# Performance work log

Measured on AMD Instinct MI355X. Metric: run time of the kernel, lower is better.

The kernel has to match this reference:

```python
import jax, jax.numpy as jnp
import numpy as np

B, S, HID = 2, 1024, 2048
NH, NKV, D = 16, 8, 128
EPS = 1e-4 / 65535.0  # observer eps from ConcatObserver


def _ste(x, dq):
    # straight-through estimator used by torch fake-quant
    return x + jax.lax.stop_gradient(dq - x)


def _fq_range(x, mn, mx):
    # 16-bit per-tensor affine quantize-dequantize over a given range
    scale = jnp.maximum((mx - mn) / 65535.0, EPS)
    zp = jnp.round(-mn / scale)
    q = jnp.clip(jnp.round(x / scale) + zp, 0.0, 65535.0)
    return _ste(x, (q - zp) * scale)


def fq16(x):
    # ActivationQDQ(bits=16), per-tensor affine, zero included in range
    mn = jnp.minimum(jnp.min(x), 0.0)
    mx = jnp.maximum(jnp.max(x), 0.0)
    return _fq_range(x, mn, mx)


def fq8_sym(x):
    # ActivationQDQ(bits=8, per_tensor_symmetric)
    scale = jnp.maximum(jnp.max(jnp.abs(x)) / 127.0, 1e-12)
    q = jnp.clip(jnp.round(x / scale), -128.0, 127.0)
    return _ste(x, q * scale)


def lpbq_linear(x, W, block=32, qmax=7.0):
    # QLinearLPBQ: int4 weights with per-(out, block-of-32-inputs) scales, no bias
    O, I = W.shape
    Wb = W.reshape(O, I // block, block)
    s = jnp.maximum(jnp.max(jnp.abs(Wb), axis=-1, keepdims=True) / qmax, 1e-12)
    Wq = (jnp.clip(jnp.round(Wb / s), -qmax - 1.0, qmax) * s).reshape(O, I)
    return x @ _ste(W, Wq).T


def rmsnorm_fq(x, w, eps=1e-6):
    # QRMSNorm(head_dim, quant_bits=16)
    var = jnp.mean(x * x, axis=-1, keepdims=True)
    return fq16(x * jax.lax.rsqrt(var + eps) * w)


def rotate_half_fq(x):
    # rotate_half with neg-half QDQ and concat observer (range = union of observed tensors)
    d = x.shape[-1] // 2
    x1, x2 = x[..., :d], x[..., d:]
    neg = fq16(-x2)
    mn = jnp.minimum(jnp.minimum(jnp.min(x), jnp.min(neg)), 0.0)
    mx = jnp.maximum(jnp.maximum(jnp.max(x), jnp.max(neg)), 0.0)
    return _fq_range(jnp.concatenate([neg, x1], axis=-1), mn, mx)


def _attn_forward(hidden_states, cos, sin, attention_mask, Wq, Wk, Wv, Wo, q_norm_w, k_norm_w):
    scaling = D ** -0.5
    hs = fq16(hidden_states)                                            # q_proj_input_qdq
    q = fq16(lpbq_linear(hs, Wq)).reshape(B, S, NH, D)                  # q_norm_input_qdq
    q = jnp.transpose(rmsnorm_fq(q, q_norm_w), (0, 2, 1, 3))            # [B,NH,S,D]
    k = fq16(lpbq_linear(hs, Wk)).reshape(B, S, NKV, D)                 # k_norm_input_qdq
    k = jnp.transpose(rmsnorm_fq(k, k_norm_w), (0, 2, 1, 3))            # [B,NKV,S,D]
    v = jnp.transpose(lpbq_linear(hs, Wv).reshape(B, S, NKV, D), (0, 2, 1, 3))
    q = fq16(q)                                                         # q_norm_output_qdq
    k = fq16(k)                                                         # k_norm_output_qdq
    c = cos[:, None, :, :]
    s_ = sin[:, None, :, :]
    q = fq16(fq16(q * c) + fq16(rotate_half_fq(q) * s_))                # q RoPE with QDQs
    k = fq16(fq16(k * c) + fq16(rotate_half_fq(k) * s_))                # k RoPE with QDQs
    k = fq8_sym(k)                                                      # k_cast_to_int8_qdq
    v = fq8_sym(fq16(v))                                                # v int16 then int8 QDQ
    k = jnp.repeat(k, NH // NKV, axis=1)                                # repeat_kv
    v = jnp.repeat(v, NH // NKV, axis=1)
    sc = fq16(jnp.full((1,), scaling, dtype=hs.dtype))                  # scaling_qdq
    attn = fq16(fq16(jnp.einsum('bhsd,bhtd->bhst', q, k)) * sc)         # qk_matmul + mul_0
    amin = fq16(jnp.min(attn, axis=-1, keepdims=True))                  # reduce_min_output_qdq
    vv = fq16(amin + fq16(jnp.full((1,), -20.0, dtype=hs.dtype)))       # minus_0 (+ neg_20)
    attn = fq16(jnp.where(attention_mask == 0, attn, vv))               # where_attn_qdq
    attn = fq16(jax.nn.softmax(attn.astype(jnp.float32), axis=-1).astype(hs.dtype))
    out = fq16(jnp.einsum('bhst,bhtd->bhsd', attn, v))                  # attn_value_matmul
    out = jnp.transpose(out, (0, 2, 1, 3)).reshape(B, S, NH * D)
    return lpbq_linear(out, Wo), attn


def setup_inputs() -> dict:
    key = jax.random.key(0)
    ks = jax.random.split(key, 6)
    hidden_states = jax.random.normal(ks[0], (B, S, HID), jnp.float32)
    pos = jnp.arange(S, dtype=jnp.float32)
    inv_freq = 1.0 / (1e6 ** (jnp.arange(0, D, 2, dtype=jnp.float32) / D))
    fr = pos[:, None] * inv_freq[None, :]
    emb = jnp.concatenate([fr, fr], axis=-1)                            # [S, D]
    cos = jnp.broadcast_to(jnp.cos(emb)[None], (B, S, D))
    sin = jnp.broadcast_to(jnp.sin(emb)[None], (B, S, D))
    attention_mask = jnp.triu(jnp.ones((S, S), jnp.int32), 1)[None, None]  # 0=keep (causal)
    Wq = jax.random.normal(ks[1], (NH * D, HID), jnp.float32) * 0.02
    Wk = jax.random.normal(ks[2], (NKV * D, HID), jnp.float32) * 0.02
    Wv = jax.random.normal(ks[3], (NKV * D, HID), jnp.float32) * 0.02
    Wo = jax.random.normal(ks[4], (HID, NH * D), jnp.float32) * 0.02
    q_norm_w = jnp.ones((D,), jnp.float32)
    k_norm_w = jnp.ones((D,), jnp.float32)
    return {"hidden_states": hidden_states, "cos": cos, "sin": sin,
            "attention_mask": attention_mask, "Wq": Wq, "Wk": Wk, "Wv": Wv, "Wo": Wo,
            "q_norm_w": q_norm_w, "k_norm_w": k_norm_w}


def reference(hidden_states, cos, sin, attention_mask, Wq, Wk, Wv, Wo, q_norm_w, k_norm_w):
    return _attn_forward(hidden_states, cos, sin, attention_mask, Wq, Wk, Wv, Wo, q_norm_w, k_norm_w)
```

## Files before the change

### kernel.cpp

```cpp
#include <hip/hip_runtime.h>
#include <cfloat>
#include <cmath>


#define FQ_EPS      1.5259021896696422e-09f
#define SCALING_F   0.08838834764831845f
#define S_LEN       1024

typedef _Float16 h8_t __attribute__((ext_vector_type(8)));
typedef _Float16 h4_t __attribute__((ext_vector_type(4)));
typedef float    f4_t __attribute__((ext_vector_type(4)));
typedef unsigned short u16x4 __attribute__((ext_vector_type(4)));

__device__ __forceinline__ unsigned f2o(float f){
  unsigned u = __float_as_uint(f);
  return (u & 0x80000000u) ? ~u : (u | 0x80000000u);
}
__device__ __forceinline__ float o2f(unsigned u){
  return __uint_as_float((u & 0x80000000u) ? (u ^ 0x80000000u) : ~u);
}
__device__ __forceinline__ float dec_slot(const unsigned* st, int s){ return o2f(st[s*16]); }

struct FQP { float scale, zp, inv; };
__device__ __forceinline__ FQP fqp_raw(float mn, float mx){
  FQP p; p.scale = fmaxf((mx - mn)/65535.0f, FQ_EPS); p.zp = rintf(-mn/p.scale);
  p.inv = 1.0f/p.scale; return p;
}
__device__ __forceinline__ FQP fqp(float mn0, float mx0){
  return fqp_raw(fminf(mn0, 0.0f), fmaxf(mx0, 0.0f));
}
__device__ __forceinline__ float fqa(float x, FQP p){
  float q = rintf(x*p.inv) + p.zp;
  q = fminf(fmaxf(q, 0.0f), 65535.0f);
  return (q - p.zp)*p.scale;
}
__device__ __forceinline__ float fq8(float x, float s, float si){
  return fminf(fmaxf(rintf(x*si), -128.0f), 127.0f)*s;
}

__device__ __forceinline__ float bred_min(float v, float* red){
  int tid = threadIdx.x; red[tid] = v; __syncthreads();
  for (int s = 128; s > 0; s >>= 1){ if (tid < s) red[tid] = fminf(red[tid], red[tid+s]); __syncthreads(); }
  float r = red[0]; __syncthreads(); return r;
}
__device__ __forceinline__ float bred_max(float v, float* red){
  int tid = threadIdx.x; red[tid] = v; __syncthreads();
  for (int s = 128; s > 0; s >>= 1){ if (tid < s) red[tid] = fmaxf(red[tid], red[tid+s]); __syncthreads(); }
  float r = red[0]; __syncthreads(); return r;
}


__global__ void k_init(unsigned* stats){
  int i = blockIdx.x*blockDim.x + threadIdx.x;
  if (i < 1024) stats[i] = (((i & 15) == 0) && (((i >> 4) & 1) == 0)) ? 0xFFFFFFFFu : 0u;
}

__global__ __launch_bounds__(256) void k_quantw4(const float* __restrict__ Wq, const float* __restrict__ Wk,
                                                 const float* __restrict__ Wv, const float* __restrict__ Wo,
                                                 _Float16* __restrict__ Qh, _Float16* __restrict__ Kh,
                                                 _Float16* __restrict__ Vh, _Float16* __restrict__ Oh){
  int bx = blockIdx.x;
  const float* W; _Float16* Wh; int base;
  if (bx < 4096){ W = Wq; Wh = Qh; base = 0; }
  else if (bx < 6144){ W = Wk; Wh = Kh; base = 4096; }
  else if (bx < 8192){ W = Wv; Wh = Vh; base = 6144; }
  else { W = Wo; Wh = Oh; base = 8192; }
  int i = (bx - base)*256 + threadIdx.x;
  float4 v = ((const float4*)W)[i];
  float am = fmaxf(fmaxf(fabsf(v.x), fabsf(v.y)), fmaxf(fabsf(v.z), fabsf(v.w)));
  #pragma unroll
  for (int m = 1; m < 8; m <<= 1) am = fmaxf(am, __shfl_xor(am, m, 64));
  float s = fmaxf(am/7.0f, 1e-12f), si = 1.0f/s;
  h4_t o;
  o[0] = (_Float16)(fminf(fmaxf(rintf(v.x*si), -8.0f), 7.0f)*s);
  o[1] = (_Float16)(fminf(fmaxf(rintf(v.y*si), -8.0f), 7.0f)*s);
  o[2] = (_Float16)(fminf(fmaxf(rintf(v.z*si), -8.0f), 7.0f)*s);
  o[3] = (_Float16)(fminf(fmaxf(rintf(v.w*si), -8.0f), 7.0f)*s);
  *(h4_t*)(Wh + ((size_t)i << 2)) = o;
}

__global__ __launch_bounds__(256) void k_minmax(const float* __restrict__ x, int n, unsigned* stats, int slot){
  float mn = FLT_MAX, mx = -FLT_MAX;
  for (int i = blockIdx.x*256 + threadIdx.x; i < n; i += gridDim.x*256){
    float v = x[i]; mn = fminf(mn, v); mx = fmaxf(mx, v);
  }
  __shared__ float red[256];
  float bmn = bred_min(mn, red), bmx = bred_max(mx, red);
  if (threadIdx.x == 0){ atomicMin(&stats[slot*16], f2o(bmn)); atomicMax(&stats[(slot+1)*16], f2o(bmx)); }
}

__global__ __launch_bounds__(256) void k_fq_ew16(const float* __restrict__ x, _Float16* __restrict__ y,
                                                 const unsigned* stats, int slot){
  FQP p = fqp(dec_slot(stats, slot), dec_slot(stats, slot+1));
  int i = blockIdx.x*256 + threadIdx.x;
  float4 v = ((const float4*)x)[i];
  h4_t o;
  o[0] = (_Float16)fqa(v.x, p); o[1] = (_Float16)fqa(v.y, p);
  o[2] = (_Float16)fqa(v.z, p); o[3] = (_Float16)fqa(v.w, p);
  *(h4_t*)(y + ((size_t)i << 2)) = o;
}

__global__ __launch_bounds__(256) void k_fq_qk(const float* __restrict__ qbuf, const float* __restrict__ kbuf,
                                               _Float16* __restrict__ q_h, _Float16* __restrict__ k_h,
                                               const unsigned* stats){
  int bx = blockIdx.x;
  if (bx < 4096){
    FQP p = fqp(dec_slot(stats, 24), dec_slot(stats, 25));
    int i = bx*256 + threadIdx.x;
    float4 v = ((const float4*)qbuf)[i];
    h4_t o;
    o[0] = (_Float16)fqa(v.x, p); o[1] = (_Float16)fqa(v.y, p);
    o[2] = (_Float16)fqa(v.z, p); o[3] = (_Float16)fqa(v.w, p);
    *(h4_t*)(q_h + ((size_t)i << 2)) = o;
  } else {
    FQP p = fqp(dec_slot(stats, 26), dec_slot(stats, 27));
    float lo = fqa(dec_slot(stats, 26), p), hi = fqa(dec_slot(stats, 27), p);
    float s8 = fmaxf(fmaxf(fabsf(lo), fabsf(hi))/127.0f, 1e-12f), s8i = 1.0f/s8;
    int i = (bx - 4096)*256 + threadIdx.x;
    float4 v = ((const float4*)kbuf)[i];
    h4_t o;
    o[0] = (_Float16)fq8(fqa(v.x, p), s8, s8i); o[1] = (_Float16)fq8(fqa(v.y, p), s8, s8i);
    o[2] = (_Float16)fq8(fqa(v.z, p), s8, s8i); o[3] = (_Float16)fq8(fqa(v.w, p), s8, s8i);
    *(h4_t*)(k_h + ((size_t)i << 2)) = o;
  }
}

#define GLDS16(g, l) __builtin_amdgcn_global_load_lds( \
    (__attribute__((address_space(1))) unsigned int*)(g), \
    (__attribute__((address_space(3))) unsigned int*)(l), 16, 0, 0)

__device__ __forceinline__ void stage_tile(const _Float16* __restrict__ src, int ld, int k0,
                                           _Float16* __restrict__ dst){
  #pragma unroll
  for (int it = 0; it < 2; it++){
    int c = threadIdx.x + (it << 8);
    int row = c >> 2, off = (c & 3) << 3;
    GLDS16(src + (size_t)row*ld + k0 + off, dst + (c << 3));
  }
}

__device__ __forceinline__ void hgemm_main(const _Float16* __restrict__ A, int lda,
                                           const _Float16* __restrict__ B, int ldb, int K,
                                           f4_t acc[4][4], _Float16* As, _Float16* Bs){
  int lane = threadIdx.x & 63, wave = threadIdx.x >> 6;
  int wm = wave & 1, wn = wave >> 1, quad = lane >> 4, l15 = lane & 15;
  for (int k0 = 0; k0 < K; k0 += 32){
    __syncthreads();
    stage_tile(A, lda, k0, As);
    stage_tile(B, ldb, k0, Bs);
    __syncthreads();
    h8_t af[4], bf[4];
    #pragma unroll
    for (int mt = 0; mt < 4; mt++)
      af[mt] = *(const h8_t*)(As + ((((wm<<6) + (mt<<4) + l15)) << 5) + (quad << 3));
    #pragma unroll
    for (int nt = 0; nt < 4; nt++)
      bf[nt] = *(const h8_t*)(Bs + ((((wn<<6) + (nt<<4) + l15)) << 5) + (quad << 3));
    #pragma unroll
    for (int mt = 0; mt < 4; mt++)
      #pragma unroll
      for (int nt = 0; nt < 4; nt++)
        acc[mt][nt] = __builtin_amdgcn_mfma_f32_16x16x32_f16(af[mt], bf[nt], acc[mt][nt], 0, 0, 0);
  }
}

#define HG_PROLOG  \
  __shared__ __align__(16) _Float16 As[4096], Bs[4096]; \
  __shared__ float red[256]; \
  f4_t acc[4][4]; \
  { f4_t zz = {0.f,0.f,0.f,0.f}; \
    for (int i=0;i<4;i++) for (int j=0;j<4;j++) acc[i][j] = zz; } \
  int lane = threadIdx.x & 63, wave = threadIdx.x >> 6; \
  int wm = wave & 1, wn = wave >> 1, quad = lane >> 4, l15 = lane & 15; (void)red; (void)lane;


__global__ __launch_bounds__(256) void k_hgemm_qkv(const _Float16* __restrict__ A,
                                                   const _Float16* __restrict__ Bq,
                                                   const _Float16* __restrict__ Bk,
                                                   const _Float16* __restrict__ Bv,
                                                   float* __restrict__ Cq, float* __restrict__ Ck,
                                                   float* __restrict__ Cv,
                                                   int K, unsigned* stats){
  HG_PROLOG
  int z = blockIdx.z;
  const _Float16* Bmat; float* C; int slotC, N, cbase;
  if (z < 2){ Bmat = Bq + (((size_t)z << 10))*K; C = Cq; slotC = 2; N = 2048; cbase = z << 10; }
  else if (z == 2){ Bmat = Bk; C = Ck; slotC = 4; N = 1024; cbase = 0; }
  else { Bmat = Bv; C = Cv; slotC = 6; N = 1024; cbase = 0; }
  int bm = blockIdx.y << 7, bn = blockIdx.x << 7;
  hgemm_main(A + (size_t)bm*K, K, Bmat + (size_t)bn*K, K, K, acc, As, Bs);
  float mn = FLT_MAX, mx = -FLT_MAX;
  #pragma unroll
  for (int mt = 0; mt < 4; mt++)
    #pragma unroll
    for (int nt = 0; nt < 4; nt++){
      int Cc = cbase + bn + (wn<<6) + (nt<<4) + l15;
      #pragma unroll
      for (int i = 0; i < 4; i++){
        int R = bm + (wm<<6) + (mt<<4) + (quad<<2) + i;
        float v = acc[mt][nt][i];
        C[(size_t)R*N + Cc] = v;
        mn = fminf(mn, v); mx = fmaxf(mx, v);
      }
    }
  float bmn = bred_min(mn, red), bmx = bred_max(mx, red);
  if (threadIdx.x == 0){ atomicMin(&stats[slotC*16], f2o(bmn)); atomicMax(&stats[(slotC+1)*16], f2o(bmx)); }
}

__global__ __launch_bounds__(256) void k_hgemm_o(const _Float16* __restrict__ A,
                                                 const _Float16* __restrict__ B,
                                                 float* __restrict__ C){
  __shared__ __align__(16) _Float16 As[4096], Bs[2048];
  f4_t acc[4][2];
  { f4_t zz = {0.f,0.f,0.f,0.f};
    for (int i = 0; i < 4; i++) for (int j = 0; j < 2; j++) acc[i][j] = zz; }
  int lane = threadIdx.x & 63, wave = threadIdx.x >> 6;
  int wm = wave & 1, wn = wave >> 1, quad = lane >> 4, l15 = lane & 15;
  int bm = blockIdx.y << 7, bn = blockIdx.x << 6;
  const _Float16* Ab = A + (size_t)bm*2048;
  const _Float16* Bb = B + (size_t)bn*2048;
  for (int k0 = 0; k0 < 2048; k0 += 32){
    __syncthreads();
    stage_tile(Ab, 2048, k0, As);
    { int c = threadIdx.x;
      int row = c >> 2, off = (c & 3) << 3;
      GLDS16(Bb + (size_t)row*2048 + k0 + off, Bs + (c << 3)); }
    __syncthreads();
    h8_t af[4], bf[2];
    #pragma unroll
    for (int mt = 0; mt < 4; mt++)
      af[mt] = *(const h8_t*)(As + ((((wm<<6) + (mt<<4) + l15)) << 5) + (quad << 3));
    #pragma unroll
    for (int nt = 0; nt < 2; nt++)
      bf[nt] = *(const h8_t*)(Bs + ((((wn<<5) + (nt<<4) + l15)) << 5) + (quad << 3));
    #pragma unroll
    for (int mt = 0; mt < 4; mt++)
      #pragma unroll
      for (int nt = 0; nt < 2; nt++)
        acc[mt][nt] = __builtin_amdgcn_mfma_f32_16x16x32_f16(af[mt], bf[nt], acc[mt][nt], 0, 0, 0);
  }
  #pragma unroll
  for (int mt = 0; mt < 4; mt++)
    #pragma unroll
    for (int nt = 0; nt < 2; nt++){
      int Cc = bn + (wn<<5) + (nt<<4) + l15;
      #pragma unroll
      for (int i = 0; i < 4; i++){
        int R = bm + (wm<<6) + (mt<<4) + (quad<<2) + i;
        C[(size_t)R*2048 + Cc] = acc[mt][nt][i];
      }
    }
}


#define QK_IDS \
  int lane = threadIdx.x & 63, wn = threadIdx.x >> 6; \
  int quad = lane >> 4, l15 = lane & 15; \
  int tid = threadIdx.x; (void)tid; (void)lane;

__device__ __forceinline__ void qk_load_a(const _Float16* __restrict__ Ab, int quad, int l15,
                                          h8_t Aq[2][4]){
  #pragma unroll
  for (int mt = 0; mt < 2; mt++)
    #pragma unroll
    for (int k0 = 0; k0 < 4; k0++)
      Aq[mt][k0] = *(const h8_t*)(Ab + (size_t)((mt<<4) + l15)*128 + (k0<<5) + (quad<<3));
}

__device__ __forceinline__ void qk_chunk32(const h8_t Aq[2][4], const _Float16* __restrict__ Kb,
                                           int bn, int wn, int quad, int l15, f4_t acc[2][2]){
  #pragma unroll
  for (int k0 = 0; k0 < 4; k0++){
    h8_t bf[2];
    #pragma unroll
    for (int nt = 0; nt < 2; nt++)
      bf[nt] = *(const h8_t*)(Kb + (size_t)(bn + (wn<<5) + (nt<<4) + l15)*128 + (k0<<5) + (quad<<3));
    #pragma unroll
    for (int mt = 0; mt < 2; mt++)
      #pragma unroll
      for (int nt = 0; nt < 2; nt++)
        acc[mt][nt] = __builtin_amdgcn_mfma_f32_16x16x32_f16(Aq[mt][k0], bf[nt], acc[mt][nt], 0, 0, 0);
  }
}

__global__ __launch_bounds__(256) void k_qk_stats(const _Float16* __restrict__ q_h, const _Float16* __restrict__ k_h,
                                                  unsigned* stats, unsigned* rowmin, unsigned* rowmax){
  QK_IDS
  int bm = blockIdx.x << 5, z = blockIdx.y;
  int b = z >> 4, h = z & 15;
  const _Float16* Ab = q_h + (size_t)z*131072 + (size_t)bm*128;
  const _Float16* Kb = k_h + (size_t)(b*8 + (h>>1))*131072;
  h8_t Aq[2][4];
  qk_load_a(Ab, quad, l15, Aq);
  float rmv[2][4], rxa[2][4], rxv[2][4];
  #pragma unroll
  for (int mt = 0; mt < 2; mt++)
    #pragma unroll
    for (int i = 0; i < 4; i++){ rmv[mt][i] = FLT_MAX; rxa[mt][i] = -FLT_MAX; rxv[mt][i] = -FLT_MAX; }
  for (int bn = 0; bn < 1024; bn += 128){
    f4_t acc[2][2];
    { f4_t zz = {0.f,0.f,0.f,0.f}; for (int i=0;i<2;i++) for (int j=0;j<2;j++) acc[i][j]=zz; }
    qk_chunk32(Aq, Kb, bn, wn, quad, l15, acc);
    #pragma unroll
    for (int mt = 0; mt < 2; mt++){
      int rb = bm + (mt<<4) + (quad<<2);
      #pragma unroll
      for (int nt = 0; nt < 2; nt++){
        int t = bn + (wn<<5) + (nt<<4) + l15;
        #pragma unroll
        for (int i = 0; i < 4; i++){
          float v = acc[mt][nt][i];
          rmv[mt][i] = fminf(rmv[mt][i], v);
          rxa[mt][i] = fmaxf(rxa[mt][i], v);
          if (t <= rb + i) rxv[mt][i] = fmaxf(rxv[mt][i], v);
        }
      }
    }
  }
  #pragma unroll
  for (int d = 1; d < 16; d <<= 1)
    #pragma unroll
    for (int mt = 0; mt < 2; mt++)
      #pragma unroll
      for (int i = 0; i < 4; i++){
        rmv[mt][i] = fminf(rmv[mt][i], __shfl_xor(rmv[mt][i], d, 64));
        rxa[mt][i] = fmaxf(rxa[mt][i], __shfl_xor(rxa[mt][i], d, 64));
        rxv[mt][i] = fmaxf(rxv[mt][i], __shfl_xor(rxv[mt][i], d, 64));
      }
  __shared__ float rminS[4][32], rmaxS[4][32];
  if (l15 == 0){
    #pragma unroll
    for (int mt = 0; mt < 2; mt++)
      #pragma unroll
      for (int i = 0; i < 4; i++){
        int rl = (mt<<4) + (quad<<2) + i;
        rminS[wn][rl] = rmv[mt][i];
        rmaxS[wn][rl] = rxv[mt][i];
      }
  }
  __syncthreads();
  if (tid < 32){
    float a = fminf(fminf(rminS[0][tid], rminS[1][tid]), fminf(rminS[2][tid], rminS[3][tid]));
    float c = fmaxf(fmaxf(rmaxS[0][tid], rmaxS[1][tid]), fmaxf(rmaxS[2][tid], rmaxS[3][tid]));
    rowmin[(z << 10) + bm + tid] = f2o(a);
    rowmax[(z << 10) + bm + tid] = f2o(c);
  }
  float mn = FLT_MAX, mx = -FLT_MAX, mxU = -FLT_MAX;
  #pragma unroll
  for (int mt = 0; mt < 2; mt++)
    #pragma unroll
    for (int i = 0; i < 4; i++){
      mn = fminf(mn, rmv[mt][i]);
      mx = fmaxf(mx, rxa[mt][i]);
      mxU = fmaxf(mxU, rxv[mt][i]);
    }
  __shared__ float red[256];
  float bmn = bred_min(mn, red), bmx = bred_max(mx, red), bmU = bred_max(mxU, red);
  if (tid == 0){
    atomicMin(&stats[28*16], f2o(bmn));
    atomicMax(&stats[29*16], f2o(bmx));
    atomicMax(&stats[31*16], f2o(bmU));
  }
}

__global__ __launch_bounds__(256) void k_rowstat_m2(const unsigned* __restrict__ rowmin, unsigned* stats, int n){
  float lm = -FLT_MAX;
  for (int i = blockIdx.x*256 + threadIdx.x; i < n; i += gridDim.x*256) lm = fmaxf(lm, o2f(rowmin[i]));
  __shared__ float red[256];
  float m = bred_max(lm, red);
  if (threadIdx.x == 0) atomicMax(&stats[35*16], f2o(m));
}
__global__ __launch_bounds__(256) void k_denom_min(const float* __restrict__ denomS, unsigned* stats, int n){
  float lm = FLT_MAX;
  for (int i = blockIdx.x*256 + threadIdx.x; i < n; i += gridDim.x*256) lm = fminf(lm, denomS[i]);
  __shared__ float red[256];
  float m = -bred_max(-lm, red);
  if (threadIdx.x == 0) atomicMin(&stats[32*16], f2o(m));
}

struct LogitQ { FQP f1, f2, fam, fvv, f3; float sc, c20; };
__device__ LogitQ derive_logit(const unsigned* st){
  LogitQ L;
  FQP ps = fqp(SCALING_F, SCALING_F); L.sc = fqa(SCALING_F, ps);
  FQP p20 = fqp(-20.0f, -20.0f);      L.c20 = fqa(-20.0f, p20);
  float gmn = dec_slot(st, 28), gmx = dec_slot(st, 29);
  float gU = dec_slot(st, 31), M2 = dec_slot(st, 35);
  L.f1 = fqp(gmn, gmx);
  float l1lo = fqa(gmn, L.f1), l1hi = fqa(gmx, L.f1);
  L.f2 = fqp(l1lo*L.sc, l1hi*L.sc);
  float amlo = fqa(fqa(gmn, L.f1)*L.sc, L.f2);
  float amhi = fqa(fqa(M2, L.f1)*L.sc, L.f2);
  L.fam = fqp(amlo, amhi);
  float vslo = fqa(amlo, L.fam) + L.c20, vshi = fqa(amhi, L.fam) + L.c20;
  L.fvv = fqp(vslo, vshi);
  float mn3 = fqa(vslo, L.fvv);
  float mx3 = fqa(fqa(gU, L.f1)*L.sc, L.f2);
  L.f3 = fqp(mn3, mx3);
  return L;
}
__device__ __forceinline__ float chainU(float raw, const LogitQ& L){
  return fqa(fqa(fqa(raw, L.f1)*L.sc, L.f2), L.f3);
}

__global__ __launch_bounds__(256) void k_qk_denom(const _Float16* __restrict__ q_h, const _Float16* __restrict__ k_h,
                                                  const unsigned* __restrict__ rowmin,
                                                  const unsigned* __restrict__ rowmax,
                                                  float* __restrict__ denomS,
                                                  unsigned short* __restrict__ q3buf,
                                                  const unsigned* stats){
  QK_IDS
  int j = blockIdx.x, z = blockIdx.y;
  int b = z >> 4, h = z & 15;
  LogitQ L = derive_logit(stats);
  const _Float16* Kb = k_h + (size_t)(b*8 + (h>>1))*131072;
  __shared__ float mRow[32], vvRow[32], vvLev[32];
  __shared__ float dS[4][32];
  for (int g = 0; g < 2; g++){
    int r = g ? (31 - j) : j;
    int bm = r << 5;
    int nch = (r >> 2) + 1;
    int cstar = (r >> 2) << 7;
    int aa = r >> 2, bb2 = r & 3;
    int cum = (aa + 1)*(2*aa + bb2);
    unsigned short* Qu = q3buf + ((size_t)z*144 + cum)*4096;
    __syncthreads();
    if (tid < 32){
      int row = (z << 10) + bm + tid;
      mRow[tid] = chainU(o2f(rowmax[row]), L);
      float tr = fqa(fqa(o2f(rowmin[row]), L.f1)*L.sc, L.f2);
      float w = fqa(fqa(tr, L.fam) + L.c20, L.fvv);
      float lv = fminf(fmaxf(rintf(w*L.f3.inv) + L.f3.zp, 0.0f), 65535.0f);
      vvLev[tid] = lv;
      vvRow[tid] = (lv - L.f3.zp)*L.f3.scale;
    }
    const _Float16* Ab = q_h + (size_t)z*131072 + (size_t)bm*128;
    h8_t Aq[2][4];
    qk_load_a(Ab, quad, l15, Aq);
    __syncthreads();
    float rs[2][4];
    #pragma unroll
    for (int mt = 0; mt < 2; mt++)
      #pragma unroll
      for (int i = 0; i < 4; i++) rs[mt][i] = 0.0f;
    for (int bn = 0; bn < (nch << 7); bn += 128){
      f4_t acc[2][2];
      { f4_t zz = {0.f,0.f,0.f,0.f}; for (int i=0;i<2;i++) for (int jj=0;jj<2;jj++) acc[i][jj]=zz; }
      qk_chunk32(Aq, Kb, bn, wn, quad, l15, acc);
      unsigned short* Qc = Qu + (size_t)(bn >> 7)*4096;
      if (bn < cstar){
        #pragma unroll
        for (int mt = 0; mt < 2; mt++){
          #pragma unroll
          for (int nt = 0; nt < 2; nt++){
            int cl = (wn<<5) + (nt<<4) + l15;
            #pragma unroll
            for (int i = 0; i < 4; i++){
              int rl = (mt<<4) + (quad<<2) + i;
              float a2 = fqa(fqa(acc[mt][nt][i], L.f1)*L.sc, L.f2);
              float lvl = fminf(fmaxf(rintf(a2*L.f3.inv) + L.f3.zp, 0.0f), 65535.0f);
              Qc[rl*128 + cl] = (unsigned short)lvl;
              float a3 = (lvl - L.f3.zp)*L.f3.scale;
              rs[mt][i] += __expf(a3 - mRow[rl]);
            }
          }
        }
      } else {
        #pragma unroll
        for (int mt = 0; mt < 2; mt++){
          #pragma unroll
          for (int nt = 0; nt < 2; nt++){
            int cl = (wn<<5) + (nt<<4) + l15;
            int t = bn + cl;
            #pragma unroll
            for (int i = 0; i < 4; i++){
              int rl = (mt<<4) + (quad<<2) + i;
              float a2 = fqa(fqa(acc[mt][nt][i], L.f1)*L.sc, L.f2);
              float lvl = fminf(fmaxf(rintf(a2*L.f3.inv) + L.f3.zp, 0.0f), 65535.0f);
              float qs = (t <= bm + rl) ? lvl : vvLev[rl];
              Qc[rl*128 + cl] = (unsigned short)qs;
              float a3 = (qs - L.f3.zp)*L.f3.scale;
              rs[mt][i] += __expf(a3 - mRow[rl]);
            }
          }
        }
      }
    }
    #pragma unroll
    for (int d = 1; d < 16; d <<= 1)
      #pragma unroll
      for (int mt = 0; mt < 2; mt++)
        #pragma unroll
        for (int i = 0; i < 4; i++) rs[mt][i] += __shfl_xor(rs[mt][i], d, 64);
    if (l15 == 0){
      #pragma unroll
      for (int mt = 0; mt < 2; mt++)
        #pragma unroll
        for (int i = 0; i < 4; i++) dS[wn][(mt<<4) + (quad<<2) + i] = rs[mt][i];
    }
    __syncthreads();
    if (tid < 32){
      float nMask = (float)(1024 - (nch << 7));
      denomS[(z << 10) + bm + tid] = (dS[0][tid] + dS[1][tid]) + (dS[2][tid] + dS[3][tid])
                                     + nMask*__expf(vvRow[tid] - mRow[tid]);
    }
  }
}

__global__ __launch_bounds__(256) void k_qk_pv(const unsigned short* __restrict__ q3buf,
                                               const _Float16* __restrict__ vT,
                                               float* __restrict__ ctx,
                                               const unsigned* __restrict__ rowmax,
                                               const float* __restrict__ denomS, unsigned* stats){
  QK_IDS
  int j = blockIdx.x, z = blockIdx.y;
  int b = z >> 4, h = z & 15;
  LogitQ L = derive_logit(stats);
  FQP p4 = fqp(0.0f, 1.0f/dec_slot(stats, 32));
  float c1024 = p4.scale*1024.0f;
  float zp3 = L.f3.zp, s3 = L.f3.scale;
  const _Float16* Vb = vT + (size_t)(b*8 + (h>>1))*131072;
  float* Cb = ctx + ((size_t)b << 10)*2048 + (size_t)h*128;
  float cmn = FLT_MAX, cmx = -FLT_MAX;
  for (int g = 0; g < 2; g++){
    int r = g ? (31 - j) : j;
    int bm = r << 5;
    int nch = (r >> 2) + 1;
    int aa = r >> 2, bb2 = r & 3;
    int cum = (aa + 1)*(2*aa + bb2);
    const unsigned short* Qu = q3buf + ((size_t)z*144 + cum)*4096;
    float mR[2], rpR[2];
    #pragma unroll
    for (int mt = 0; mt < 2; mt++){
      int row = (z << 10) + bm + (mt<<4) + l15;
      mR[mt] = chainU(o2f(rowmax[row]), L);
      rpR[mt] = p4.inv/denomS[row];
    }
    f4_t pacc[2][2];
    { f4_t zz = {0.f,0.f,0.f,0.f}; for (int i=0;i<2;i++) for (int jj=0;jj<2;jj++) pacc[i][jj]=zz; }
    for (int c = 0; c < nch; c++){
      const unsigned short* Qc = Qu + (size_t)c*4096;
      #pragma unroll
      for (int k0 = 0; k0 < 4; k0++){
        h8_t af[2], bf[2];
        #pragma unroll
        for (int mt = 0; mt < 2; mt++){
          const unsigned short* pr = Qc + ((mt<<4) + l15)*128 + (k0<<5) + (quad<<3);
          u16x4 u = *(const u16x4*)pr, w = *(const u16x4*)(pr + 4);
          h8_t o;
          #pragma unroll
          for (int jj = 0; jj < 4; jj++){
            float a3u = ((float)u[jj] - zp3)*s3;
            float nu = fminf(fmaxf(rintf(__expf(a3u - mR[mt])*rpR[mt]), 0.0f), 65535.0f);
            o[jj] = (_Float16)(nu*c1024);
            float a3w = ((float)w[jj] - zp3)*s3;
            float nw = fminf(fmaxf(rintf(__expf(a3w - mR[mt])*rpR[mt]), 0.0f), 65535.0f);
            o[jj+4] = (_Float16)(nw*c1024);
          }
          af[mt] = o;
        }
        #pragma unroll
        for (int nt = 0; nt < 2; nt++)
          bf[nt] = *(const h8_t*)(Vb + (size_t)((wn<<5) + (nt<<4) + l15)*1024 + (c<<7) + (k0<<5) + (quad<<3));
        #pragma unroll
        for (int mt = 0; mt < 2; mt++)
          #pragma unroll
          for (int nt = 0; nt < 2; nt++)
            pacc[mt][nt] = __builtin_amdgcn_mfma_f32_16x16x32_f16(af[mt], bf[nt], pacc[mt][nt], 0, 0, 0);
      }
    }
    #pragma unroll
    for (int mt = 0; mt < 2; mt++)
      #pragma unroll
      for (int nt = 0; nt < 2; nt++){
        int Cc = (wn<<5) + (nt<<4) + l15;
        #pragma unroll
        for (int i = 0; i < 4; i++){
          int R = bm + (mt<<4) + (quad<<2) + i;
          float v = pacc[mt][nt][i]*(1.0f/1024.0f);
          Cb[(size_t)R*2048 + Cc] = v;
          cmn = fminf(cmn, v); cmx = fmaxf(cmx, v);
        }
      }
  }
  __shared__ float red[256];
  float bmn = bred_min(cmn, red), bmx = bred_max(cmx, red);
  if (tid == 0){ atomicMin(&stats[36*16], f2o(bmn)); atomicMax(&stats[37*16], f2o(bmx)); }
}

__global__ __launch_bounds__(256) void k_attn_expand(const unsigned short* __restrict__ q3buf,
                                                     float* __restrict__ attn,
                                                     const unsigned* __restrict__ rowmax,
                                                     const float* __restrict__ denomS,
                                                     const unsigned* stats){
  int c = blockIdx.x, r = blockIdx.y, z = blockIdx.z;
  int nch = (r >> 2) + 1;
  int tid = threadIdx.x;
  float* Cb = attn + ((size_t)z << 20) + ((size_t)(r << 5))*1024 + (c << 7);
  if (c >= nch){
    f4_t zz = {0.f,0.f,0.f,0.f};
    #pragma unroll
    for (int it = 0; it < 4; it++){
      int idx = (it << 8) + tid;
      int row = idx >> 5, col = (idx & 31) << 2;
      __builtin_nontemporal_store(zz, (f4_t*)(Cb + (size_t)row*1024 + col));
    }
    return;
  }
  LogitQ L = derive_logit(stats);
  FQP p4 = fqp(0.0f, 1.0f/dec_slot(stats, 32));
  float zp3 = L.f3.zp, s3 = L.f3.scale;
  int aa = r >> 2, bb2 = r & 3;
  int cum = (aa + 1)*(2*aa + bb2);
  const unsigned short* Qu = q3buf + ((size_t)z*144 + cum + c)*4096;
  #pragma unroll
  for (int it = 0; it < 4; it++){
    int idx = (it << 8) + tid;
    int row = idx >> 5, col = (idx & 31) << 2;
    int grow = (z << 10) + (r << 5) + row;
    float m = chainU(o2f(rowmax[grow]), L);
    float rp = p4.inv/denomS[grow];
    u16x4 u = *(const u16x4*)(Qu + row*128 + col);
    f4_t v4;
    #pragma unroll
    for (int jj = 0; jj < 4; jj++){
      float a3 = ((float)u[jj] - zp3)*s3;
      float n = fminf(fmaxf(rintf(__expf(a3 - m)*rp), 0.0f), 65535.0f);
      v4[jj] = n*p4.scale;
    }
    __builtin_nontemporal_store(v4, (f4_t*)(Cb + (size_t)row*1024 + col));
  }
}


__global__ __launch_bounds__(256) void k_rms(const float* __restrict__ lin, float* __restrict__ buf,
                                             const float* __restrict__ gw, unsigned* stats,
                                             int slot_lin, int slot_out, int NHh, int rows){
  FQP pA = fqp(dec_slot(stats, slot_lin), dec_slot(stats, slot_lin+1));
  int lane = threadIdx.x & 63;
  int wv = (blockIdx.x*256 + threadIdx.x) >> 6;
  int nwv = (gridDim.x*256) >> 6;
  float w0 = gw[lane], w1 = gw[lane + 64];
  float fmn = FLT_MAX, fmx = -FLT_MAX, hmn = FLT_MAX, hmx = -FLT_MAX;
  for (int r = wv; r < rows; r += nwv){
    int h = r % NHh; int rem = r / NHh; int s2 = rem & 1023; int b = rem >> 10;
    const float* src = lin + (size_t)r*128;
    float x0 = fqa(src[lane], pA), x1 = fqa(src[lane + 64], pA);
    float ss = x0*x0 + x1*x1;
    #pragma unroll
    for (int m = 1; m < 64; m <<= 1) ss += __shfl_xor(ss, m, 64);
    float rr = 1.0f/sqrtf(ss*(1.0f/128.0f) + 1e-6f);
    float y0 = x0*rr*w0, y1 = x1*rr*w1;
    float* dst = buf + ((size_t)((b*NHh + h) << 10) + s2)*128;
    dst[lane] = y0; dst[lane + 64] = y1;
    fmn = fminf(fmn, fminf(y0, y1)); fmx = fmaxf(fmx, fmaxf(y0, y1));
    hmn = fminf(hmn, y1); hmx = fmaxf(hmx, y1);
  }
  __shared__ float red[256];
  float a = bred_min(fmn, red), bb = bred_max(fmx, red);
  float c = bred_min(hmn, red), d = bred_max(hmx, red);
  if (threadIdx.x == 0){
    atomicMin(&stats[slot_out*16], f2o(a));     atomicMax(&stats[(slot_out+1)*16], f2o(bb));
    atomicMin(&stats[(slot_out+2)*16], f2o(c)); atomicMax(&stats[(slot_out+3)*16], f2o(d));
  }
}

struct RopeQ { FQP B, C, E, F; };
__device__ RopeQ derive_rope(const unsigned* st, int base){
  float ymn = dec_slot(st, base),   ymx = dec_slot(st, base+1);
  float y2mn = dec_slot(st, base+2), y2mx = dec_slot(st, base+3);
  RopeQ r;
  r.B = fqp(ymn, ymx);
  float zmn = fqa(ymn, r.B), zmx = fqa(ymx, r.B);
  r.C = fqp(zmn, zmx);
  float zlo = fqa(zmn, r.C), zhi = fqa(zmx, r.C);
  float z2lo = fqa(fqa(y2mn, r.B), r.C), z2hi = fqa(fqa(y2mx, r.B), r.C);
  r.E = fqp(-z2hi, -z2lo);
  float nlo = fqa(-z2hi, r.E), nhi = fqa(-z2lo, r.E);
  r.F = fqp_raw(fminf(fminf(zlo, nlo), 0.0f), fmaxf(fmaxf(zhi, nhi), 0.0f));
  return r;
}

__global__ __launch_bounds__(256) void k_rope(float* __restrict__ bufq, float* __restrict__ bufk,
                                              const float* __restrict__ cosp, const float* __restrict__ sinp,
                                              unsigned* stats, int do_write){
  int isK = (blockIdx.x >= 1024);
  float* buf = isK ? bufk : bufq;
  int slot_norm = isK ? 12 : 8, slot_prod = isK ? 20 : 16, slot_sum = isK ? 26 : 24;
  int NHh = isK ? 8 : 16, rows = isK ? 16384 : 32768;
  int bid = isK ? (blockIdx.x - 1024) : blockIdx.x;
  int nblk = isK ? 512 : 1024;
  RopeQ R = derive_rope(stats, slot_norm);
  FQP pD, pG;
  if (do_write){
    pD = fqp(dec_slot(stats, slot_prod),   dec_slot(stats, slot_prod+1));
    pG = fqp(dec_slot(stats, slot_prod+2), dec_slot(stats, slot_prod+3));
  }
  int lane = threadIdx.x & 63;
  int wv = (bid*256 + threadIdx.x) >> 6, nwv = (nblk*256) >> 6;
  float m0 = FLT_MAX, M0 = -FLT_MAX, m1 = FLT_MAX, M1 = -FLT_MAX;
  for (int r = wv; r < rows; r += nwv){
    int s2 = r & 1023; int bh = r >> 10; int b = bh/NHh;
    float* base = buf + (size_t)r*128;
    float y0 = base[lane], y1 = base[lane + 64];
    float z0 = fqa(fqa(y0, R.B), R.C), z1 = fqa(fqa(y1, R.B), R.C);
    const float* cr = cosp + (size_t)((b << 10) + s2)*128;
    const float* sr = sinp + (size_t)((b << 10) + s2)*128;
    float c0 = cr[lane], c1 = cr[lane + 64], sn0 = sr[lane], sn1 = sr[lane + 64];
    float pc0 = z0*c0, pc1 = z1*c1;
    float rh0 = fqa(fqa(-z1, R.E), R.F);
    float rh1 = fqa(z0, R.F);
    float ps0 = rh0*sn0, ps1 = rh1*sn1;
    if (!do_write){
      m0 = fminf(m0, fminf(pc0, pc1)); M0 = fmaxf(M0, fmaxf(pc0, pc1));
      m1 = fminf(m1, fminf(ps0, ps1)); M1 = fmaxf(M1, fmaxf(ps0, ps1));
    } else {
      float sv0 = fqa(pc0, pD) + fqa(ps0, pG);
      float sv1 = fqa(pc1, pD) + fqa(ps1, pG);
      base[lane] = sv0; base[lane + 64] = sv1;
      m0 = fminf(m0, fminf(sv0, sv1)); M0 = fmaxf(M0, fmaxf(sv0, sv1));
    }
  }
  __shared__ float red[256];
  if (!do_write){
    float a = bred_min(m0, red), bb = bred_max(M0, red);
    float c = bred_min(m1, red), d = bred_max(M1, red);
    if (threadIdx.x == 0){
      atomicMin(&stats[slot_prod*16], f2o(a));     atomicMax(&stats[(slot_prod+1)*16], f2o(bb));
      atomicMin(&stats[(slot_prod+2)*16], f2o(c)); atomicMax(&stats[(slot_prod+3)*16], f2o(d));
    }
  } else {
    float a = bred_min(m0, red), bb = bred_max(M0, red);
    if (threadIdx.x == 0){ atomicMin(&stats[slot_sum*16], f2o(a)); atomicMax(&stats[(slot_sum+1)*16], f2o(bb)); }
  }
}

__global__ __launch_bounds__(256) void k_vT(const float* __restrict__ vlin, _Float16* __restrict__ vT,
                                            const unsigned* stats){
  FQP pv = fqp(dec_slot(stats, 6), dec_slot(stats, 7));
  float vlo = fqa(dec_slot(stats, 6), pv), vhi = fqa(dec_slot(stats, 7), pv);
  float v8s = fmaxf(fmaxf(fabsf(vlo), fabsf(vhi))/127.0f, 1e-12f), v8si = 1.0f/v8s;
  __shared__ float tile[64][65];
  int bkv = blockIdx.z, t0 = blockIdx.x << 6, d0 = blockIdx.y << 6;
  int b = bkv >> 3, kv = bkv & 7;
  const float* src = vlin + ((size_t)(b << 10))*1024 + (size_t)kv*128;
  int tx = threadIdx.x & 63, tq = threadIdx.x >> 6;
  #pragma unroll
  for (int i = 0; i < 16; i++){
    int tt = (i << 2) + tq;
    float x = src[(size_t)(t0 + tt)*1024 + d0 + tx];
    tile[tx][tt] = fq8(fqa(x, pv), v8s, v8si);
  }
  __syncthreads();
  _Float16* dst = vT + (size_t)bkv*131072;
  #pragma unroll
  for (int i = 0; i < 16; i++){
    int dd = (i << 2) + tq;
    dst[(size_t)(d0 + dd)*1024 + t0 + tx] = (_Float16)tile[dd][tx];
  }
}

extern "C" void kernel_launch(void* const* d_in, const int* in_sizes, int n_in,
                              void* d_out, int out_size, void* d_ws, size_t ws_size,
                              hipStream_t stream){
  (void)in_sizes; (void)n_in; (void)out_size; (void)ws_size;
  const float* hs   = (const float*)d_in[0];
  const float* cosp = (const float*)d_in[1];
  const float* sinp = (const float*)d_in[2];
  const float* Wq   = (const float*)d_in[4];
  const float* Wk   = (const float*)d_in[5];
  const float* Wv   = (const float*)d_in[6];
  const float* Wo   = (const float*)d_in[7];
  const float* qnw  = (const float*)d_in[8];
  const float* knw  = (const float*)d_in[9];

  float* outp = (float*)d_out;
  float* attn = outp + 4194304;

  const size_t MEG = 1u << 20;
  float* wsf = (float*)d_ws;
  _Float16* woq_h = (_Float16*)(wsf + 0);
  _Float16* wqq_h = (_Float16*)(wsf + 2*MEG);
  _Float16* wkq_h = (_Float16*)(wsf + 4*MEG);
  _Float16* wvq_h = (_Float16*)(wsf + 5*MEG);
  _Float16* hsq_h = (_Float16*)(wsf + 6*MEG);
  float* qlin = wsf + 8*MEG;  float* ctx = qlin;
  float* klin = wsf + 12*MEG;
  float* vlin = wsf + 14*MEG;
  float* qbuf = wsf + 16*MEG;
  float* kbuf = wsf + 20*MEG;
  _Float16* q_h   = (_Float16*)(wsf + 22*MEG);
  _Float16* k_h   = (_Float16*)(wsf + 24*MEG);
  _Float16* vT_h  = (_Float16*)(wsf + 25*MEG);
  _Float16* ctx_h = (_Float16*)(wsf + 26*MEG);
  unsigned* rowmin = (unsigned*)(wsf + 28*MEG);
  unsigned* rowmax = (unsigned*)(wsf + 28*MEG + 32768);
  float* denomS = wsf + 28*MEG + 65536;
  unsigned* stats = (unsigned*)(wsf + 28*MEG + 98304);
  unsigned short* q3buf = (unsigned short*)(wsf + 12*MEG);

  k_init<<<4, 256, 0, stream>>>(stats);

  k_quantw4<<<12288, 256, 0, stream>>>(Wq, Wk, Wv, Wo, wqq_h, wkq_h, wvq_h, woq_h);

  k_minmax<<<1024, 256, 0, stream>>>(hs, 4194304, stats, 0);
  k_fq_ew16<<<4096, 256, 0, stream>>>(hs, hsq_h, stats, 0);

  k_hgemm_qkv<<<dim3(8, 16, 4), 256, 0, stream>>>(hsq_h, wqq_h, wkq_h, wvq_h,
                                                  qlin, klin, vlin, 2048, stats);

  k_rms<<<1024, 256, 0, stream>>>(qlin, qbuf, qnw, stats, 2, 8, 16, 32768);
  k_rms<<<512, 256, 0, stream>>>(klin, kbuf, knw, stats, 4, 12, 8, 16384);

  k_rope<<<1536, 256, 0, stream>>>(qbuf, kbuf, cosp, sinp, stats, 0);
  k_rope<<<1536, 256, 0, stream>>>(qbuf, kbuf, cosp, sinp, stats, 1);

  k_fq_qk<<<6144, 256, 0, stream>>>(qbuf, kbuf, q_h, k_h, stats);
  k_vT<<<dim3(16, 2, 16), 256, 0, stream>>>(vlin, vT_h, stats);

  k_qk_stats<<<dim3(32, 32), 256, 0, stream>>>(q_h, k_h, stats, rowmin, rowmax);
  k_rowstat_m2<<<8, 256, 0, stream>>>(rowmin, stats, 32768);
  k_qk_denom<<<dim3(16, 32), 256, 0, stream>>>(q_h, k_h, rowmin, rowmax, denomS, q3buf, stats);
  k_denom_min<<<8, 256, 0, stream>>>(denomS, stats, 32768);
  k_qk_pv<<<dim3(16, 32), 256, 0, stream>>>(q3buf, vT_h, ctx, rowmax, denomS, stats);
  k_attn_expand<<<dim3(8, 32, 32), 256, 0, stream>>>(q3buf, attn, rowmax, denomS, stats);

  k_fq_ew16<<<4096, 256, 0, stream>>>(ctx, ctx_h, stats, 36);
  k_hgemm_o<<<dim3(32, 16), 256, 0, stream>>>(ctx_h, woq_h, outp);
}
```

Measured before the change: 595.3 us.

## Fuse minmax, row-stat and denom reductions into producers; write attn in PV; K=64 GEMM steps

Folds the hidden-state min/max reduction into extra blocks of the weight-quant kernel. It moves the rowmin-max and denom-min reductions into warp shuffles plus atomics inside the producing kernels, dropping two tiny launches. The PV kernel now writes the dequantized attention probabilities directly, replacing the separate expand kernel with a zero-fill kernel that only covers the masked region. Both GEMMs stage 64-wide K slices per sync, which halves barrier count but doubles LDS per block and may lower occupancy.

Measured after the change: 589.6 us. No clear change (-1.0%).

```diff
diff --git a/kernel.cpp b/kernel.cpp
--- a/kernel.cpp
+++ b/kernel.cpp
@@ -58,8 +58,19 @@
 __global__ __launch_bounds__(256) void k_quantw4(const float* __restrict__ Wq, const float* __restrict__ Wk,
                                                  const float* __restrict__ Wv, const float* __restrict__ Wo,
                                                  _Float16* __restrict__ Qh, _Float16* __restrict__ Kh,
-                                                 _Float16* __restrict__ Vh, _Float16* __restrict__ Oh){
+                                                 _Float16* __restrict__ Vh, _Float16* __restrict__ Oh,
+                                                 const float* __restrict__ hs, unsigned* stats){
   int bx = blockIdx.x;
+  if (bx >= 12288){
+    float mn = FLT_MAX, mx = -FLT_MAX;
+    for (int i = (bx - 12288)*256 + threadIdx.x; i < 4194304; i += 262144){
+      float v = hs[i]; mn = fminf(mn, v); mx = fmaxf(mx, v);
+    }
+    __shared__ float red[256];
+    float bmn = bred_min(mn, red), bmx = bred_max(mx, red);
+    if (threadIdx.x == 0){ atomicMin(&stats[0], f2o(bmn)); atomicMax(&stats[16], f2o(bmx)); }
+    return;
+  }
   const float* W; _Float16* Wh; int base;
   if (bx < 4096){ W = Wq; Wh = Qh; base = 0; }
   else if (bx < 6144){ W = Wk; Wh = Kh; base = 4096; }
@@ -77,16 +88,6 @@
   o[2] = (_Float16)(fminf(fmaxf(rintf(v.z*si), -8.0f), 7.0f)*s);
   o[3] = (_Float16)(fminf(fmaxf(rintf(v.w*si), -8.0f), 7.0f)*s);
   *(h4_t*)(Wh + ((size_t)i << 2)) = o;
-}
-
-__global__ __launch_bounds__(256) void k_minmax(const float* __restrict__ x, int n, unsigned* stats, int slot){
-  float mn = FLT_MAX, mx = -FLT_MAX;
-  for (int i = blockIdx.x*256 + threadIdx.x; i < n; i += gridDim.x*256){
-    float v = x[i]; mn = fminf(mn, v); mx = fmaxf(mx, v);
-  }
-  __shared__ float red[256];
-  float bmn = bred_min(mn, red), bmx = bred_max(mx, red);
-  if (threadIdx.x == 0){ atomicMin(&stats[slot*16], f2o(bmn)); atomicMax(&stats[(slot+1)*16], f2o(bmx)); }
 }
 
 __global__ __launch_bounds__(256) void k_fq_ew16(const float* __restrict__ x, _Float16* __restrict__ y,
@@ -139,39 +140,38 @@
   }
 }
 
-__device__ __forceinline__ void hgemm_main(const _Float16* __restrict__ A, int lda,
-                                           const _Float16* __restrict__ B, int ldb, int K,
-                                           f4_t acc[4][4], _Float16* As, _Float16* Bs){
+__device__ __forceinline__ void hgemm_main64(const _Float16* __restrict__ A, int lda,
+                                             const _Float16* __restrict__ B, int ldb, int K,
+                                             f4_t acc[4][4], _Float16* As, _Float16* As2,
+                                             _Float16* Bs, _Float16* Bs2){
   int lane = threadIdx.x & 63, wave = threadIdx.x >> 6;
   int wm = wave & 1, wn = wave >> 1, quad = lane >> 4, l15 = lane & 15;
-  for (int k0 = 0; k0 < K; k0 += 32){
+  for (int k0 = 0; k0 < K; k0 += 64){
     __syncthreads();
     stage_tile(A, lda, k0, As);
+    stage_tile(A, lda, k0 + 32, As2);
     stage_tile(B, ldb, k0, Bs);
+    stage_tile(B, ldb, k0 + 32, Bs2);
     __syncthreads();
-    h8_t af[4], bf[4];
-    #pragma unroll
-    for (int mt = 0; mt < 4; mt++)
-      af[mt] = *(const h8_t*)(As + ((((wm<<6) + (mt<<4) + l15)) << 5) + (quad << 3));
-    #pragma unroll
-    for (int nt = 0; nt < 4; nt++)
-      bf[nt] = *(const h8_t*)(Bs + ((((wn<<6) + (nt<<4) + l15)) << 5) + (quad << 3));
-    #pragma unroll
-    for (int mt = 0; mt < 4; mt++)
+    #pragma unroll
+    for (int half = 0; half < 2; half++){
+      const _Float16* Ah = half ? As2 : As;
+      const _Float16* Bh = half ? Bs2 : Bs;
+      h8_t af[4], bf[4];
+      #pragma unroll
+      for (int mt = 0; mt < 4; mt++)
+        af[mt] = *(const h8_t*)(Ah + ((((wm<<6) + (mt<<4) + l15)) << 5) + (quad << 3));
       #pragma unroll
       for (int nt = 0; nt < 4; nt++)
-        acc[mt][nt] = __builtin_amdgcn_mfma_f32_16x16x32_f16(af[mt], bf[nt], acc[mt][nt], 0, 0, 0);
-  }
-}
-
-#define HG_PROLOG  \
-  __shared__ __align__(16) _Float16 As[4096], Bs[4096]; \
-  __shared__ float red[256]; \
-  f4_t acc[4][4]; \
-  { f4_t zz = {0.f,0.f,0.f,0.f}; \
-    for (int i=0;i<4;i++) for (int j=0;j<4;j++) acc[i][j] = zz; } \
-  int lane = threadIdx.x & 63, wave = threadIdx.x >> 6; \
-  int wm = wave & 1, wn = wave >> 1, quad = lane >> 4, l15 = lane & 15; (void)red; (void)lane;
+        bf[nt] = *(const h8_t*)(Bh + ((((wn<<6) + (nt<<4) + l15)) << 5) + (quad << 3));
+      #pragma unroll
+      for (int mt = 0; mt < 4; mt++)
+        #pragma unroll
+        for (int nt = 0; nt < 4; nt++)
+          acc[mt][nt] = __builtin_amdgcn_mfma_f32_16x16x32_f16(af[mt], bf[nt], acc[mt][nt], 0, 0, 0);
+    }
+  }
+}
 
 
 __global__ __launch_bounds__(256) void k_hgemm_qkv(const _Float16* __restrict__ A,
@@ -181,14 +181,20 @@
                                                    float* __restrict__ Cq, float* __restrict__ Ck,
                                                    float* __restrict__ Cv,
                                                    int K, unsigned* stats){
-  HG_PROLOG
+  __shared__ __align__(16) _Float16 As[4096], As2[4096], Bs[4096], Bs2[4096];
+  __shared__ float red[256];
+  f4_t acc[4][4];
+  { f4_t zz = {0.f,0.f,0.f,0.f};
+    for (int i=0;i<4;i++) for (int j=0;j<4;j++) acc[i][j] = zz; }
+  int lane = threadIdx.x & 63, wave = threadIdx.x >> 6;
+  int wm = wave & 1, wn = wave >> 1, quad = lane >> 4, l15 = lane & 15; (void)lane;
   int z = blockIdx.z;
   const _Float16* Bmat; float* C; int slotC, N, cbase;
   if (z < 2){ Bmat = Bq + (((size_t)z << 10))*K; C = Cq; slotC = 2; N = 2048; cbase = z << 10; }
   else if (z == 2){ Bmat = Bk; C = Ck; slotC = 4; N = 1024; cbase = 0; }
   else { Bmat = Bv; C = Cv; slotC = 6; N = 1024; cbase = 0; }
   int bm = blockIdx.y << 7, bn = blockIdx.x << 7;
-  hgemm_main(A + (size_t)bm*K, K, Bmat + (size_t)bn*K, K, K, acc, As, Bs);
+  hgemm_main64(A + (size_t)bm*K, K, Bmat + (size_t)bn*K, K, K, acc, As, As2, Bs, Bs2);
   float mn = FLT_MAX, mx = -FLT_MAX;
   #pragma unroll
   for (int mt = 0; mt < 4; mt++)
@@ -210,7 +216,7 @@
 __global__ __launch_bounds__(256) void k_hgemm_o(const _Float16* __restrict__ A,
                                                  const _Float16* __restrict__ B,
                                                  float* __restrict__ C){
-  __shared__ __align__(16) _Float16 As[4096], Bs[2048];
+  __shared__ __align__(16) _Float16 As[4096], As2[4096], Bs[2048], Bs2[2048];
   f4_t acc[4][2];
   { f4_t zz = {0.f,0.f,0.f,0.f};
     for (int i = 0; i < 4; i++) for (int j = 0; j < 2; j++) acc[i][j] = zz; }
@@ -219,25 +225,32 @@
   int bm = blockIdx.y << 7, bn = blockIdx.x << 6;
   const _Float16* Ab = A + (size_t)bm*2048;
   const _Float16* Bb = B + (size_t)bn*2048;
-  for (int k0 = 0; k0 < 2048; k0 += 32){
+  for (int k0 = 0; k0 < 2048; k0 += 64){
     __syncthreads();
     stage_tile(Ab, 2048, k0, As);
+    stage_tile(Ab, 2048, k0 + 32, As2);
     { int c = threadIdx.x;
       int row = c >> 2, off = (c & 3) << 3;
-      GLDS16(Bb + (size_t)row*2048 + k0 + off, Bs + (c << 3)); }
+      GLDS16(Bb + (size_t)row*2048 + k0 + off, Bs + (c << 3));
+      GLDS16(Bb + (size_t)row*2048 + k0 + 32 + off, Bs2 + (c << 3)); }
     __syncthreads();
-    h8_t af[4], bf[2];
-    #pragma unroll
-    for (int mt = 0; mt < 4; mt++)
-      af[mt] = *(const h8_t*)(As + ((((wm<<6) + (mt<<4) + l15)) << 5) + (quad << 3));
-    #pragma unroll
-    for (int nt = 0; nt < 2; nt++)
-      bf[nt] = *(const h8_t*)(Bs + ((((wn<<5) + (nt<<4) + l15)) << 5) + (quad << 3));
-    #pragma unroll
-    for (int mt = 0; mt < 4; mt++)
+    #pragma unroll
+    for (int half = 0; half < 2; half++){
+      const _Float16* Ah = half ? As2 : As;
+      const _Float16* Bh = half ? Bs2 : Bs;
+      h8_t af[4], bf[2];
+      #pragma unroll
+      for (int mt = 0; mt < 4; mt++)
+        af[mt] = *(const h8_t*)(Ah + ((((wm<<6) + (mt<<4) + l15)) << 5) + (quad << 3));
       #pragma unroll
       for (int nt = 0; nt < 2; nt++)
-        acc[mt][nt] = __builtin_amdgcn_mfma_f32_16x16x32_f16(af[mt], bf[nt], acc[mt][nt], 0, 0, 0);
+        bf[nt] = *(const h8_t*)(Bh + ((((wn<<5) + (nt<<4) + l15)) << 5) + (quad << 3));
+      #pragma unroll
+      for (int mt = 0; mt < 4; mt++)
+        #pragma unroll
+        for (int nt = 0; nt < 2; nt++)
+          acc[mt][nt] = __builtin_amdgcn_mfma_f32_16x16x32_f16(af[mt], bf[nt], acc[mt][nt], 0, 0, 0);
+    }
   }
   #pragma unroll
   for (int mt = 0; mt < 4; mt++)
@@ -344,6 +357,10 @@
     float c = fmaxf(fmaxf(rmaxS[0][tid], rmaxS[1][tid]), fmaxf(rmaxS[2][tid], rmaxS[3][tid]));
     rowmin[(z << 10) + bm + tid] = f2o(a);
     rowmax[(z << 10) + bm + tid] = f2o(c);
+    float am = a;
+    #pragma unroll
+    for (int d = 1; d < 32; d <<= 1) am = fmaxf(am, __shfl_xor(am, d, 32));
+    if (tid == 0) atomicMax(&stats[35*16], f2o(am));
   }
   float mn = FLT_MAX, mx = -FLT_MAX, mxU = -FLT_MAX;
   #pragma unroll
@@ -361,21 +378,6 @@
     atomicMax(&stats[29*16], f2o(bmx));
     atomicMax(&stats[31*16], f2o(bmU));
   }
-}
-
-__global__ __launch_bounds__(256) void k_rowstat_m2(const unsigned* __restrict__ rowmin, unsigned* stats, int n){
-  float lm = -FLT_MAX;
-  for (int i = blockIdx.x*256 + threadIdx.x; i < n; i += gridDim.x*256) lm = fmaxf(lm, o2f(rowmin[i]));
-  __shared__ float red[256];
-  float m = bred_max(lm, red);
-  if (threadIdx.x == 0) atomicMax(&stats[35*16], f2o(m));
-}
-__global__ __launch_bounds__(256) void k_denom_min(const float* __restrict__ denomS, unsigned* stats, int n){
-  float lm = FLT_MAX;
-  for (int i = blockIdx.x*256 + threadIdx.x; i < n; i += gridDim.x*256) lm = fminf(lm, denomS[i]);
-  __shared__ float red[256];
-  float m = -bred_max(-lm, red);
-  if (threadIdx.x == 0) atomicMin(&stats[32*16], f2o(m));
 }
 
 struct LogitQ { FQP f1, f2, fam, fvv, f3; float sc, c20; };
@@ -407,7 +409,7 @@
                                                   const unsigned* __restrict__ rowmax,
                                                   float* __restrict__ denomS,
                                                   unsigned short* __restrict__ q3buf,
-                                                  const unsigned* stats){
+                                                  unsigned* stats){
   QK_IDS
   int j = blockIdx.x, z = blockIdx.y;
   int b = z >> 4, h = z & 15;
@@ -500,15 +502,20 @@
     __syncthreads();
     if (tid < 32){
       float nMask = (float)(1024 - (nch << 7));
-      denomS[(z << 10) + bm + tid] = (dS[0][tid] + dS[1][tid]) + (dS[2][tid] + dS[3][tid])
-                                     + nMask*__expf(vvRow[tid] - mRow[tid]);
+      float ds = (dS[0][tid] + dS[1][tid]) + (dS[2][tid] + dS[3][tid])
+                 + nMask*__expf(vvRow[tid] - mRow[tid]);
+      denomS[(z << 10) + bm + tid] = ds;
+      float dm = ds;
+      #pragma unroll
+      for (int d = 1; d < 32; d <<= 1) dm = fminf(dm, __shfl_xor(dm, d, 32));
+      if (tid == 0) atomicMin(&stats[32*16], f2o(dm));
     }
   }
 }
 
 __global__ __launch_bounds__(256) void k_qk_pv(const unsigned short* __restrict__ q3buf,
                                                const _Float16* __restrict__ vT,
-                                               float* __restrict__ ctx,
+                                               float* __restrict__ ctx, float* __restrict__ attn,
                                                const unsigned* __restrict__ rowmax,
                                                const float* __restrict__ denomS, unsigned* stats){
   QK_IDS
@@ -517,6 +524,7 @@
   LogitQ L = derive_logit(stats);
   FQP p4 = fqp(0.0f, 1.0f/dec_slot(stats, 32));
   float c1024 = p4.scale*1024.0f;
+  float p4s = p4.scale;
   float zp3 = L.f3.zp, s3 = L.f3.scale;
   const _Float16* Vb = vT + (size_t)(b*8 + (h>>1))*131072;
   float* Cb = ctx + ((size_t)b << 10)*2048 + (size_t)h*128;
@@ -528,6 +536,7 @@
     int aa = r >> 2, bb2 = r & 3;
     int cum = (aa + 1)*(2*aa + bb2);
     const unsigned short* Qu = q3buf + ((size_t)z*144 + cum)*4096;
+    float* Ap = attn + ((size_t)z << 20) + (size_t)bm*1024;
     float mR[2], rpR[2];
     #pragma unroll
     for (int mt = 0; mt < 2; mt++){
@@ -547,16 +556,22 @@
           const unsigned short* pr = Qc + ((mt<<4) + l15)*128 + (k0<<5) + (quad<<3);
           u16x4 u = *(const u16x4*)pr, w = *(const u16x4*)(pr + 4);
           h8_t o;
+          f4_t va, vb;
           #pragma unroll
           for (int jj = 0; jj < 4; jj++){
             float a3u = ((float)u[jj] - zp3)*s3;
             float nu = fminf(fmaxf(rintf(__expf(a3u - mR[mt])*rpR[mt]), 0.0f), 65535.0f);
             o[jj] = (_Float16)(nu*c1024);
+            va[jj] = nu*p4s;
             float a3w = ((float)w[jj] - zp3)*s3;
             float nw = fminf(fmaxf(rintf(__expf(a3w - mR[mt])*rpR[mt]), 0.0f), 65535.0f);
             o[jj+4] = (_Float16)(nw*c1024);
+            vb[jj] = nw*p4s;
           }
           af[mt] = o;
+          float* ap = Ap + (size_t)((mt<<4) + l15)*1024 + (c<<7) + (k0<<5) + (quad<<3);
+          *(f4_t*)ap = va;
+          *(f4_t*)(ap + 4) = vb;
         }
         #pragma unroll
         for (int nt = 0; nt < 2; nt++)
@@ -587,47 +602,22 @@
   if (tid == 0){ atomicMin(&stats[36*16], f2o(bmn)); atomicMax(&stats[37*16], f2o(bmx)); }
 }
 
-__global__ __launch_bounds__(256) void k_attn_expand(const unsigned short* __restrict__ q3buf,
-                                                     float* __restrict__ attn,
-                                                     const unsigned* __restrict__ rowmax,
-                                                     const float* __restrict__ denomS,
-                                                     const unsigned* stats){
-  int c = blockIdx.x, r = blockIdx.y, z = blockIdx.z;
-  int nch = (r >> 2) + 1;
-  int tid = threadIdx.x;
-  float* Cb = attn + ((size_t)z << 20) + ((size_t)(r << 5))*1024 + (c << 7);
-  if (c >= nch){
-    f4_t zz = {0.f,0.f,0.f,0.f};
-    #pragma unroll
-    for (int it = 0; it < 4; it++){
-      int idx = (it << 8) + tid;
-      int row = idx >> 5, col = (idx & 31) << 2;
-      __builtin_nontemporal_store(zz, (f4_t*)(Cb + (size_t)row*1024 + col));
-    }
-    return;
-  }
-  LogitQ L = derive_logit(stats);
-  FQP p4 = fqp(0.0f, 1.0f/dec_slot(stats, 32));
-  float zp3 = L.f3.zp, s3 = L.f3.scale;
-  int aa = r >> 2, bb2 = r & 3;
-  int cum = (aa + 1)*(2*aa + bb2);
-  const unsigned short* Qu = q3buf + ((size_t)z*144 + cum + c)*4096;
-  #pragma unroll
-  for (int it = 0; it < 4; it++){
-    int idx = (it << 8) + tid;
-    int row = idx >> 5, col = (idx & 31) << 2;
-    int grow = (z << 10) + (r << 5) + row;
-    float m = chainU(o2f(rowmax[grow]), L);
-    float rp = p4.inv/denomS[grow];
-    u16x4 u = *(const u16x4*)(Qu + row*128 + col);
-    f4_t v4;
-    #pragma unroll
-    for (int jj = 0; jj < 4; jj++){
-      float a3 = ((float)u[jj] - zp3)*s3;
-      float n = fminf(fmaxf(rintf(__expf(a3 - m)*rp), 0.0f), 65535.0f);
-      v4[jj] = n*p4.scale;
-    }
-    __builtin_nontemporal_store(v4, (f4_t*)(Cb + (size_t)row*1024 + col));
+__global__ __launch_bounds__(256) void k_attn_zero(float* __restrict__ attn){
+  int j = blockIdx.x, z = blockIdx.y;
+  int lane = threadIdx.x & 63, wn = threadIdx.x >> 6;
+  f4_t zz = {0.f,0.f,0.f,0.f};
+  #pragma unroll
+  for (int g = 0; g < 2; g++){
+    int r = g ? (31 - j) : j;
+    int nch = (r >> 2) + 1;
+    int col0 = nch << 7;
+    if (col0 >= 1024) continue;
+    float* Cb = attn + ((size_t)z << 20) + ((size_t)(r << 5))*1024;
+    for (int rr = wn; rr < 32; rr += 4){
+      float* rowp = Cb + (size_t)rr*1024;
+      for (int c = col0 + (lane << 2); c < 1024; c += 256)
+        __builtin_nontemporal_store(zz, (f4_t*)(rowp + c));
+    }
   }
 }
 
@@ -800,9 +790,8 @@
 
   k_init<<<4, 256, 0, stream>>>(stats);
 
-  k_quantw4<<<12288, 256, 0, stream>>>(Wq, Wk, Wv, Wo, wqq_h, wkq_h, wvq_h, woq_h);
-
-  k_minmax<<<1024, 256, 0, stream>>>(hs, 4194304, stats, 0);
+  k_quantw4<<<13312, 256, 0, stream>>>(Wq, Wk, Wv, Wo, wqq_h, wkq_h, wvq_h, woq_h, hs, stats);
+
   k_fq_ew16<<<4096, 256, 0, stream>>>(hs, hsq_h, stats, 0);
 
   k_hgemm_qkv<<<dim3(8, 16, 4), 256, 0, stream>>>(hsq_h, wqq_h, wkq_h, wvq_h,
@@ -818,11 +807,9 @@
   k_vT<<<dim3(16, 2, 16), 256, 0, stream>>>(vlin, vT_h, stats);
 
   k_qk_stats<<<dim3(32, 32), 256, 0, stream>>>(q_h, k_h, stats, rowmin, rowmax);
-  k_rowstat_m2<<<8, 256, 0, stream>>>(rowmin, stats, 32768);
   k_qk_denom<<<dim3(16, 32), 256, 0, stream>>>(q_h, k_h, rowmin, rowmax, denomS, q3buf, stats);
-  k_denom_min<<<8, 256, 0, stream>>>(denomS, stats, 32768);
-  k_qk_pv<<<dim3(16, 32), 256, 0, stream>>>(q3buf, vT_h, ctx, rowmax, denomS, stats);
-  k_attn_expand<<<dim3(8, 32, 32), 256, 0, stream>>>(q3buf, attn, rowmax, denomS, stats);
+  k_qk_pv<<<dim3(16, 32), 256, 0, stream>>>(q3buf, vT_h, ctx, attn, rowmax, denomS, stats);
+  k_attn_zero<<<dim3(16, 32), 256, 0, stream>>>(attn);
 
   k_fq_ew16<<<4096, 256, 0, stream>>>(ctx, ctx_h, stats, 36);
   k_hgemm_o<<<dim3(32, 16), 256, 0, stream>>>(ctx_h, woq_h, outp);
```
